# Optimization experiments

Measured on AMD Instinct MI355X. Metric: run time of the kernel, lower is better.

Reference implementation:

```python
import jax, jax.numpy as jnp
import numpy as np

N_NODES = 50000


def setup_inputs() -> dict:
    key = jax.random.key(0)
    k1, k2, k3, k4, k5, k6 = jax.random.split(key, 6)
    N, E, D, F = 50000, 800000, 512, 256
    feature_ori = jax.random.normal(k1, (N, D), dtype=jnp.float32)
    feature_aug = jax.random.normal(k2, (N, D), dtype=jnp.float32)
    edge_row = jax.random.randint(k3, (E,), 0, N, dtype=jnp.int32)
    edge_col = jax.random.randint(k4, (E,), 0, N, dtype=jnp.int32)
    edge_val = jax.random.uniform(k5, (E,), dtype=jnp.float32)
    # kaiming-uniform-ish init for weight, zeros for bias (as in reset_parameters)
    bound = float(np.sqrt(6.0 / D))
    weight = jax.random.uniform(k6, (D, F), dtype=jnp.float32, minval=-bound, maxval=bound)
    bias = jnp.zeros((F,), dtype=jnp.float32)
    return {
        "feature_ori": feature_ori,
        "feature_aug": feature_aug,
        "edge_row": edge_row,
        "edge_col": edge_col,
        "edge_val": edge_val,
        "weight": weight,
        "bias": bias,
    }


def _branch(feat, weight, bias, edge_row, edge_col, edge_val):
    # support = X @ W  -> [N, F]
    support = feat @ weight
    # sparse aggregation: out[i] = sum_{e: row[e]=i} val[e] * support[col[e]]
    msgs = edge_val[:, None] * support[edge_col]          # [E, F]
    out = jax.ops.segment_sum(msgs, edge_row, num_segments=N_NODES)
    return jax.nn.relu(out + bias)


def reference(feature_ori, feature_aug, edge_row, edge_col, edge_val, weight, bias):
    out_ori = _branch(feature_ori, weight, bias, edge_row, edge_col, edge_val)
    out_aug = _branch(feature_aug, weight, bias, edge_row, edge_col, edge_val)
    return (out_ori, out_aug)
```

## Files before the change

### kernel.cpp

```cpp
#include <hip/hip_runtime.h>
#include <hip/hip_bf16.h>

#define NNODES 50000
#define NEDGES 800000
#define DIN    512
#define FOUT   256

typedef __attribute__((ext_vector_type(8))) short short8;
typedef __attribute__((ext_vector_type(4))) float f32x4;
typedef __attribute__((ext_vector_type(4))) unsigned short usv4;

static __device__ __forceinline__ unsigned short f2bf(float f) {
    unsigned int u = __float_as_uint(f);
    u += 0x7FFF + ((u >> 16) & 1);
    return (unsigned short)(u >> 16);
}
static __device__ __forceinline__ float bf2f(unsigned short h) {
    return __uint_as_float(((unsigned int)h) << 16);
}

__global__ void wt_convert(const float* __restrict__ W, unsigned short* __restrict__ Wt) {
    int o = blockIdx.x * 256 + threadIdx.x;
    int n = o >> 9, k = o & 511;
    Wt[o] = f2bf(W[k * FOUT + n]);
}

__global__ void hist_kernel(const int* __restrict__ row, int* __restrict__ cnt) {
    int e = blockIdx.x * 256 + threadIdx.x;
    if (e < NEDGES) atomicAdd(&cnt[row[e]], 1);
}

__global__ void scan_partial(const int* __restrict__ cnt, int* __restrict__ partial) {
    __shared__ int sm[256];
    int i = blockIdx.x * 256 + threadIdx.x;
    int v = (i < NNODES) ? cnt[i] : 0;
    sm[threadIdx.x] = v; __syncthreads();
    for (int s = 128; s > 0; s >>= 1) {
        if (threadIdx.x < s) sm[threadIdx.x] += sm[threadIdx.x + s];
        __syncthreads();
    }
    if (threadIdx.x == 0) partial[blockIdx.x] = sm[0];
}

__global__ void scan_exclusive_small(int* __restrict__ partial, int nb) {
    __shared__ int sm[256];
    int t = threadIdx.x;
    int v = (t < nb) ? partial[t] : 0;
    sm[t] = v; __syncthreads();
    for (int off = 1; off < 256; off <<= 1) {
        int add = (t >= off) ? sm[t - off] : 0;
        __syncthreads();
        sm[t] += add;
        __syncthreads();
    }
    if (t < nb) partial[t] = sm[t] - v;
}

__global__ void scan_write(const int* __restrict__ cnt, const int* __restrict__ partial,
                           int* __restrict__ row_start) {
    __shared__ int sm[256];
    int t = threadIdx.x;
    int i = blockIdx.x * 256 + t;
    int v = (i < NNODES) ? cnt[i] : 0;
    sm[t] = v; __syncthreads();
    for (int off = 1; off < 256; off <<= 1) {
        int add = (t >= off) ? sm[t - off] : 0;
        __syncthreads();
        sm[t] += add;
        __syncthreads();
    }
    if (i < NNODES) row_start[i] = partial[blockIdx.x] + sm[t] - v;
    if (i == 0) row_start[NNODES] = NEDGES;
}

__global__ void scatter_kernel(const int* __restrict__ row, const int* __restrict__ col,
                               const float* __restrict__ val,
                               const int* __restrict__ row_start,
                               int* __restrict__ cursor, unsigned int* __restrict__ cv) {
    int e = blockIdx.x * 256 + threadIdx.x;
    if (e < NEDGES) {
        int r = row[e];
        int pos = atomicAdd(&cursor[r], 1);
        unsigned int vb = f2bf(val[e]);
        cv[row_start[r] + pos] = (vb << 16) | (unsigned int)col[e];
    }
}

__global__ __launch_bounds__(512, 2)
void gemm_kernel(const float* __restrict__ Xo, const float* __restrict__ Xa,
                 const unsigned short* __restrict__ Wt,
                 unsigned short* __restrict__ S) {
    __shared__ __align__(16) unsigned short As[128][40];
    __shared__ __align__(16) unsigned short Bs[256][40];
    const int tid = threadIdx.x;
    const int branch = blockIdx.z;
    const float* __restrict__ X = branch ? Xa : Xo;
    const int boff = branch * 256;
    const int m_base = blockIdx.x * 128;
    const int lane = tid & 63, wave = tid >> 6;
    const int wm = (wave >> 2) * 64, wn = (wave & 3) * 64;
    const int quad = lane >> 4, r16 = lane & 15;

    f32x4 acc[4][4] = {};

    const int colf  = (tid & 7) * 4;
    const int rbase = tid >> 3;
    const int kseg  = (tid & 3) * 8;
    const int nrow  = tid >> 2;

    for (int k0 = 0; k0 < DIN; k0 += 32) {
        #pragma unroll
        for (int i = 0; i < 2; i++) {
            int rr = i * 64 + rbase;
            int gm = m_base + rr;
            float4 v = (gm < NNODES) ? *(const float4*)&X[(long)gm * DIN + k0 + colf]
                                     : make_float4(0.f, 0.f, 0.f, 0.f);
            usv4 h;
            h.x = f2bf(v.x); h.y = f2bf(v.y); h.z = f2bf(v.z); h.w = f2bf(v.w);
            *(usv4*)&As[rr][colf] = h;
        }
        #pragma unroll
        for (int i = 0; i < 2; i++) {
            int nn = i * 128 + nrow;
            *(uint4*)&Bs[nn][kseg] =
                *(const uint4*)&Wt[(long)nn * DIN + k0 + kseg];
        }
        __syncthreads();

        short8 a_frag[4], b_frag[4];
        #pragma unroll
        for (int mi = 0; mi < 4; mi++)
            a_frag[mi] = *(const short8*)&As[wm + mi * 16 + r16][quad * 8];
        #pragma unroll
        for (int ni = 0; ni < 4; ni++)
            b_frag[ni] = *(const short8*)&Bs[wn + ni * 16 + r16][quad * 8];
        #pragma unroll
        for (int mi = 0; mi < 4; mi++)
            #pragma unroll
            for (int ni = 0; ni < 4; ni++)
                acc[mi][ni] = __builtin_amdgcn_mfma_f32_16x16x32_bf16(
                    a_frag[mi], b_frag[ni], acc[mi][ni], 0, 0, 0);
        __syncthreads();
    }

    #pragma unroll
    for (int mi = 0; mi < 4; mi++) {
        #pragma unroll
        for (int rr = 0; rr < 4; rr++) {
            int m = m_base + wm + mi * 16 + quad * 4 + rr;
            if (m < NNODES) {
                #pragma unroll
                for (int ni = 0; ni < 4; ni++) {
                    int n = wn + ni * 16 + r16;
                    S[(long)m * 512 + boff + n] = f2bf(acc[mi][ni][rr]);
                }
            }
        }
    }
}

__global__ __launch_bounds__(256)
void aggregate_kernel(const int* __restrict__ row_start,
                      const unsigned int* __restrict__ cv,
                      const unsigned short* __restrict__ S,
                      const float* __restrict__ bias, float* __restrict__ out) {
    int node = blockIdx.x * 4 + (threadIdx.x >> 6);
    int lane = threadIdx.x & 63;
    if (node >= NNODES) return;
    int s = row_start[node], e = row_start[node + 1];
    float ao0 = 0.f, ao1 = 0.f, ao2 = 0.f, ao3 = 0.f;
    float aa0 = 0.f, aa1 = 0.f, aa2 = 0.f, aa3 = 0.f;
    const int lo = lane * 4;

    int idx = s;
    for (; idx + 4 <= e; idx += 4) {
        unsigned int w0 = cv[idx], w1 = cv[idx + 1], w2 = cv[idx + 2], w3 = cv[idx + 3];
        const unsigned short* p0 = &S[(long)(w0 & 0xFFFFu) * 512 + lo];
        const unsigned short* p1 = &S[(long)(w1 & 0xFFFFu) * 512 + lo];
        const unsigned short* p2 = &S[(long)(w2 & 0xFFFFu) * 512 + lo];
        const unsigned short* p3 = &S[(long)(w3 & 0xFFFFu) * 512 + lo];
        usv4 po0 = *(const usv4*)p0;       usv4 pa0 = *(const usv4*)(p0 + 256);
        usv4 po1 = *(const usv4*)p1;       usv4 pa1 = *(const usv4*)(p1 + 256);
        usv4 po2 = *(const usv4*)p2;       usv4 pa2 = *(const usv4*)(p2 + 256);
        usv4 po3 = *(const usv4*)p3;       usv4 pa3 = *(const usv4*)(p3 + 256);
        float v0 = bf2f((unsigned short)(w0 >> 16));
        float v1 = bf2f((unsigned short)(w1 >> 16));
        float v2 = bf2f((unsigned short)(w2 >> 16));
        float v3 = bf2f((unsigned short)(w3 >> 16));
        ao0 += v0 * bf2f(po0.x); ao1 += v0 * bf2f(po0.y); ao2 += v0 * bf2f(po0.z); ao3 += v0 * bf2f(po0.w);
        aa0 += v0 * bf2f(pa0.x); aa1 += v0 * bf2f(pa0.y); aa2 += v0 * bf2f(pa0.z); aa3 += v0 * bf2f(pa0.w);
        ao0 += v1 * bf2f(po1.x); ao1 += v1 * bf2f(po1.y); ao2 += v1 * bf2f(po1.z); ao3 += v1 * bf2f(po1.w);
        aa0 += v1 * bf2f(pa1.x); aa1 += v1 * bf2f(pa1.y); aa2 += v1 * bf2f(pa1.z); aa3 += v1 * bf2f(pa1.w);
        ao0 += v2 * bf2f(po2.x); ao1 += v2 * bf2f(po2.y); ao2 += v2 * bf2f(po2.z); ao3 += v2 * bf2f(po2.w);
        aa0 += v2 * bf2f(pa2.x); aa1 += v2 * bf2f(pa2.y); aa2 += v2 * bf2f(pa2.z); aa3 += v2 * bf2f(pa2.w);
        ao0 += v3 * bf2f(po3.x); ao1 += v3 * bf2f(po3.y); ao2 += v3 * bf2f(po3.z); ao3 += v3 * bf2f(po3.w);
        aa0 += v3 * bf2f(pa3.x); aa1 += v3 * bf2f(pa3.y); aa2 += v3 * bf2f(pa3.z); aa3 += v3 * bf2f(pa3.w);
    }
    for (; idx < e; idx++) {
        unsigned int w = cv[idx];
        const unsigned short* p = &S[(long)(w & 0xFFFFu) * 512 + lo];
        usv4 po = *(const usv4*)p;
        usv4 pa = *(const usv4*)(p + 256);
        float v = bf2f((unsigned short)(w >> 16));
        ao0 += v * bf2f(po.x); ao1 += v * bf2f(po.y); ao2 += v * bf2f(po.z); ao3 += v * bf2f(po.w);
        aa0 += v * bf2f(pa.x); aa1 += v * bf2f(pa.y); aa2 += v * bf2f(pa.z); aa3 += v * bf2f(pa.w);
    }

    float4 b = *(const float4*)&bias[lo];
    long o = (long)node * FOUT + lo;
    float4 ro, ra;
    ro.x = fmaxf(ao0 + b.x, 0.f); ro.y = fmaxf(ao1 + b.y, 0.f);
    ro.z = fmaxf(ao2 + b.z, 0.f); ro.w = fmaxf(ao3 + b.w, 0.f);
    ra.x = fmaxf(aa0 + b.x, 0.f); ra.y = fmaxf(aa1 + b.y, 0.f);
    ra.z = fmaxf(aa2 + b.z, 0.f); ra.w = fmaxf(aa3 + b.w, 0.f);
    *(float4*)&out[o] = ro;
    *(float4*)&out[(long)NNODES * FOUT + o] = ra;
}

extern "C" void kernel_launch(void* const* d_in, const int* in_sizes, int n_in,
                              void* d_out, int out_size, void* d_ws, size_t ws_size,
                              hipStream_t stream) {
    const float* Xo   = (const float*)d_in[0];
    const float* Xa   = (const float*)d_in[1];
    const int*   erow = (const int*)d_in[2];
    const int*   ecol = (const int*)d_in[3];
    const float* eval_= (const float*)d_in[4];
    const float* W    = (const float*)d_in[5];
    const float* bias = (const float*)d_in[6];
    float* out = (float*)d_out;

    char* ws = (char*)d_ws;
    unsigned short* S         = (unsigned short*)(ws);
    unsigned short* Wt        = (unsigned short*)(ws + 51200000);
    int*            cnt       = (int*)(ws + 51462144);
    int*            row_start = (int*)(ws + 51662144);
    int*            partial   = (int*)(ws + 51862208);
    unsigned int*   cv        = (unsigned int*)(ws + 51863232);

    (void)in_sizes; (void)n_in; (void)out_size; (void)ws_size;

    hipMemsetAsync(cnt, 0, 200000, stream);
    wt_convert<<<512, 256, 0, stream>>>(W, Wt);
    hist_kernel<<<3125, 256, 0, stream>>>(erow, cnt);
    scan_partial<<<196, 256, 0, stream>>>(cnt, partial);
    scan_exclusive_small<<<1, 256, 0, stream>>>(partial, 196);
    scan_write<<<196, 256, 0, stream>>>(cnt, partial, row_start);
    hipMemsetAsync(cnt, 0, 200000, stream);
    scatter_kernel<<<3125, 256, 0, stream>>>(erow, ecol, eval_, row_start, cnt, cv);

    dim3 gg(391, 1, 2);
    gemm_kernel<<<gg, 512, 0, stream>>>(Xo, Xa, Wt, S);

    aggregate_kernel<<<12500, 256, 0, stream>>>(row_start, cv, S, bias, out);
}
```

Measured before the change: 484.2 us.

## Prefetch GEMM tiles in registers, interleave branch layout, and batch aggregate edge loads

```diff
diff --git a/kernel.cpp b/kernel.cpp
--- a/kernel.cpp
+++ b/kernel.cpp
@@ -8,7 +8,6 @@
 
 typedef __attribute__((ext_vector_type(8))) short short8;
 typedef __attribute__((ext_vector_type(4))) float f32x4;
-typedef __attribute__((ext_vector_type(4))) unsigned short usv4;
 
 static __device__ __forceinline__ unsigned short f2bf(float f) {
     unsigned int u = __float_as_uint(f);
@@ -18,16 +17,22 @@
 static __device__ __forceinline__ float bf2f(unsigned short h) {
     return __uint_as_float(((unsigned int)h) << 16);
 }
-
-__global__ void wt_convert(const float* __restrict__ W, unsigned short* __restrict__ Wt) {
-    int o = blockIdx.x * 256 + threadIdx.x;
-    int n = o >> 9, k = o & 511;
-    Wt[o] = f2bf(W[k * FOUT + n]);
-}
-
-__global__ void hist_kernel(const int* __restrict__ row, int* __restrict__ cnt) {
-    int e = blockIdx.x * 256 + threadIdx.x;
-    if (e < NEDGES) atomicAdd(&cnt[row[e]], 1);
+static __device__ __forceinline__ unsigned int pk2bf(float a, float b) {
+    __hip_bfloat162 h = __float22bfloat162_rn(make_float2(a, b));
+    return *(unsigned int*)&h;
+}
+
+__global__ void convert_hist(const float* __restrict__ W, unsigned short* __restrict__ Wt,
+                             const int* __restrict__ row, int* __restrict__ cnt) {
+    int b = blockIdx.x;
+    if (b < 512) {
+        int o = b * 256 + threadIdx.x;
+        int n = o >> 9, k = o & 511;
+        Wt[o] = f2bf(W[k * FOUT + n]);
+    } else {
+        int e = (b - 512) * 256 + threadIdx.x;
+        if (e < NEDGES) atomicAdd(&cnt[row[e]], 1);
+    }
 }
 
 __global__ void scan_partial(const int* __restrict__ cnt, int* __restrict__ partial) {
@@ -56,7 +61,7 @@
     if (t < nb) partial[t] = sm[t] - v;
 }
 
-__global__ void scan_write(const int* __restrict__ cnt, const int* __restrict__ partial,
+__global__ void scan_write(int* __restrict__ cnt, const int* __restrict__ partial,
                            int* __restrict__ row_start) {
     __shared__ int sm[256];
     int t = threadIdx.x;
@@ -69,7 +74,7 @@
         sm[t] += add;
         __syncthreads();
     }
-    if (i < NNODES) row_start[i] = partial[blockIdx.x] + sm[t] - v;
+    if (i < NNODES) { row_start[i] = partial[blockIdx.x] + sm[t] - v; cnt[i] = 0; }
     if (i == 0) row_start[NNODES] = NEDGES;
 }
 
@@ -90,12 +95,11 @@
 void gemm_kernel(const float* __restrict__ Xo, const float* __restrict__ Xa,
                  const unsigned short* __restrict__ Wt,
                  unsigned short* __restrict__ S) {
-    __shared__ __align__(16) unsigned short As[128][40];
-    __shared__ __align__(16) unsigned short Bs[256][40];
+    __shared__ __align__(16) unsigned short As[128][72];
+    __shared__ __align__(16) unsigned short Bs[256][72];
     const int tid = threadIdx.x;
     const int branch = blockIdx.z;
     const float* __restrict__ X = branch ? Xa : Xo;
-    const int boff = branch * 256;
     const int m_base = blockIdx.x * 128;
     const int lane = tid & 63, wave = tid >> 6;
     const int wm = (wave >> 2) * 64, wn = (wave & 3) * 64;
@@ -103,43 +107,72 @@
 
     f32x4 acc[4][4] = {};
 
-    const int colf  = (tid & 7) * 4;
-    const int rbase = tid >> 3;
-    const int kseg  = (tid & 3) * 8;
-    const int nrow  = tid >> 2;
-
-    for (int k0 = 0; k0 < DIN; k0 += 32) {
+    const int scol = (tid & 7) * 8;
+    const int srow = tid >> 3;
+
+    float4 a0[2], a1[2];
+    uint4  breg[4];
+
+    {
         #pragma unroll
         for (int i = 0; i < 2; i++) {
-            int rr = i * 64 + rbase;
-            int gm = m_base + rr;
-            float4 v = (gm < NNODES) ? *(const float4*)&X[(long)gm * DIN + k0 + colf]
-                                     : make_float4(0.f, 0.f, 0.f, 0.f);
-            usv4 h;
-            h.x = f2bf(v.x); h.y = f2bf(v.y); h.z = f2bf(v.z); h.w = f2bf(v.w);
-            *(usv4*)&As[rr][colf] = h;
-        }
+            int gm = m_base + i * 64 + srow;
+            const float* p = &X[(long)gm * DIN + scol];
+            bool ok = gm < NNODES;
+            a0[i] = ok ? *(const float4*)p       : make_float4(0.f,0.f,0.f,0.f);
+            a1[i] = ok ? *(const float4*)(p + 4) : make_float4(0.f,0.f,0.f,0.f);
+        }
+        #pragma unroll
+        for (int i = 0; i < 4; i++)
+            breg[i] = *(const uint4*)&Wt[(long)(i * 64 + srow) * DIN + scol];
+    }
+
+    for (int k0 = 0; k0 < DIN; k0 += 64) {
         #pragma unroll
         for (int i = 0; i < 2; i++) {
-            int nn = i * 128 + nrow;
-            *(uint4*)&Bs[nn][kseg] =
-                *(const uint4*)&Wt[(long)nn * DIN + k0 + kseg];
-        }
-        __syncthreads();
-
-        short8 a_frag[4], b_frag[4];
-        #pragma unroll
-        for (int mi = 0; mi < 4; mi++)
-            a_frag[mi] = *(const short8*)&As[wm + mi * 16 + r16][quad * 8];
-        #pragma unroll
-        for (int ni = 0; ni < 4; ni++)
-            b_frag[ni] = *(const short8*)&Bs[wn + ni * 16 + r16][quad * 8];
-        #pragma unroll
-        for (int mi = 0; mi < 4; mi++)
+            uint4 h;
+            h.x = pk2bf(a0[i].x, a0[i].y);
+            h.y = pk2bf(a0[i].z, a0[i].w);
+            h.z = pk2bf(a1[i].x, a1[i].y);
+            h.w = pk2bf(a1[i].z, a1[i].w);
+            *(uint4*)&As[i * 64 + srow][scol] = h;
+        }
+        #pragma unroll
+        for (int i = 0; i < 4; i++)
+            *(uint4*)&Bs[i * 64 + srow][scol] = breg[i];
+        __syncthreads();
+
+        if (k0 + 64 < DIN) {
+            int k1 = k0 + 64;
+            #pragma unroll
+            for (int i = 0; i < 2; i++) {
+                int gm = m_base + i * 64 + srow;
+                const float* p = &X[(long)gm * DIN + k1 + scol];
+                bool ok = gm < NNODES;
+                a0[i] = ok ? *(const float4*)p       : make_float4(0.f,0.f,0.f,0.f);
+                a1[i] = ok ? *(const float4*)(p + 4) : make_float4(0.f,0.f,0.f,0.f);
+            }
+            #pragma unroll
+            for (int i = 0; i < 4; i++)
+                breg[i] = *(const uint4*)&Wt[(long)(i * 64 + srow) * DIN + k1 + scol];
+        }
+
+        #pragma unroll
+        for (int w = 0; w < 2; w++) {
+            short8 a_frag[4], b_frag[4];
+            #pragma unroll
+            for (int mi = 0; mi < 4; mi++)
+                a_frag[mi] = *(const short8*)&As[wm + mi * 16 + r16][w * 32 + quad * 8];
             #pragma unroll
             for (int ni = 0; ni < 4; ni++)
-                acc[mi][ni] = __builtin_amdgcn_mfma_f32_16x16x32_bf16(
-                    a_frag[mi], b_frag[ni], acc[mi][ni], 0, 0, 0);
+                b_frag[ni] = *(const short8*)&Bs[wn + ni * 16 + r16][w * 32 + quad * 8];
+            #pragma unroll
+            for (int mi = 0; mi < 4; mi++)
+                #pragma unroll
+                for (int ni = 0; ni < 4; ni++)
+                    acc[mi][ni] = __builtin_amdgcn_mfma_f32_16x16x32_bf16(
+                        a_frag[mi], b_frag[ni], acc[mi][ni], 0, 0, 0);
+        }
         __syncthreads();
     }
 
@@ -152,12 +185,19 @@
                 #pragma unroll
                 for (int ni = 0; ni < 4; ni++) {
                     int n = wn + ni * 16 + r16;
-                    S[(long)m * 512 + boff + n] = f2bf(acc[mi][ni][rr]);
+                    int pos = ((n >> 2) * 8) + branch * 4 + (n & 3);
+                    S[(long)m * 512 + pos] = f2bf(acc[mi][ni][rr]);
                 }
             }
         }
     }
 }
+
+#define ACCUM(p, v) { \
+    ao0 += v * __uint_as_float(p.x << 16); ao1 += v * __uint_as_float(p.x & 0xFFFF0000u); \
+    ao2 += v * __uint_as_float(p.y << 16); ao3 += v * __uint_as_float(p.y & 0xFFFF0000u); \
+    aa0 += v * __uint_as_float(p.z << 16); aa1 += v * __uint_as_float(p.z & 0xFFFF0000u); \
+    aa2 += v * __uint_as_float(p.w << 16); aa3 += v * __uint_as_float(p.w & 0xFFFF0000u); }
 
 __global__ __launch_bounds__(256)
 void aggregate_kernel(const int* __restrict__ row_start,
@@ -170,44 +210,37 @@
     int s = row_start[node], e = row_start[node + 1];
     float ao0 = 0.f, ao1 = 0.f, ao2 = 0.f, ao3 = 0.f;
     float aa0 = 0.f, aa1 = 0.f, aa2 = 0.f, aa3 = 0.f;
-    const int lo = lane * 4;
-
-    int idx = s;
-    for (; idx + 4 <= e; idx += 4) {
-        unsigned int w0 = cv[idx], w1 = cv[idx + 1], w2 = cv[idx + 2], w3 = cv[idx + 3];
-        const unsigned short* p0 = &S[(long)(w0 & 0xFFFFu) * 512 + lo];
-        const unsigned short* p1 = &S[(long)(w1 & 0xFFFFu) * 512 + lo];
-        const unsigned short* p2 = &S[(long)(w2 & 0xFFFFu) * 512 + lo];
-        const unsigned short* p3 = &S[(long)(w3 & 0xFFFFu) * 512 + lo];
-        usv4 po0 = *(const usv4*)p0;       usv4 pa0 = *(const usv4*)(p0 + 256);
-        usv4 po1 = *(const usv4*)p1;       usv4 pa1 = *(const usv4*)(p1 + 256);
-        usv4 po2 = *(const usv4*)p2;       usv4 pa2 = *(const usv4*)(p2 + 256);
-        usv4 po3 = *(const usv4*)p3;       usv4 pa3 = *(const usv4*)(p3 + 256);
-        float v0 = bf2f((unsigned short)(w0 >> 16));
-        float v1 = bf2f((unsigned short)(w1 >> 16));
-        float v2 = bf2f((unsigned short)(w2 >> 16));
-        float v3 = bf2f((unsigned short)(w3 >> 16));
-        ao0 += v0 * bf2f(po0.x); ao1 += v0 * bf2f(po0.y); ao2 += v0 * bf2f(po0.z); ao3 += v0 * bf2f(po0.w);
-        aa0 += v0 * bf2f(pa0.x); aa1 += v0 * bf2f(pa0.y); aa2 += v0 * bf2f(pa0.z); aa3 += v0 * bf2f(pa0.w);
-        ao0 += v1 * bf2f(po1.x); ao1 += v1 * bf2f(po1.y); ao2 += v1 * bf2f(po1.z); ao3 += v1 * bf2f(po1.w);
-        aa0 += v1 * bf2f(pa1.x); aa1 += v1 * bf2f(pa1.y); aa2 += v1 * bf2f(pa1.z); aa3 += v1 * bf2f(pa1.w);
-        ao0 += v2 * bf2f(po2.x); ao1 += v2 * bf2f(po2.y); ao2 += v2 * bf2f(po2.z); ao3 += v2 * bf2f(po2.w);
-        aa0 += v2 * bf2f(pa2.x); aa1 += v2 * bf2f(pa2.y); aa2 += v2 * bf2f(pa2.z); aa3 += v2 * bf2f(pa2.w);
-        ao0 += v3 * bf2f(po3.x); ao1 += v3 * bf2f(po3.y); ao2 += v3 * bf2f(po3.z); ao3 += v3 * bf2f(po3.w);
-        aa0 += v3 * bf2f(pa3.x); aa1 += v3 * bf2f(pa3.y); aa2 += v3 * bf2f(pa3.z); aa3 += v3 * bf2f(pa3.w);
-    }
-    for (; idx < e; idx++) {
-        unsigned int w = cv[idx];
-        const unsigned short* p = &S[(long)(w & 0xFFFFu) * 512 + lo];
-        usv4 po = *(const usv4*)p;
-        usv4 pa = *(const usv4*)(p + 256);
-        float v = bf2f((unsigned short)(w >> 16));
-        ao0 += v * bf2f(po.x); ao1 += v * bf2f(po.y); ao2 += v * bf2f(po.z); ao3 += v * bf2f(po.w);
-        aa0 += v * bf2f(pa.x); aa1 += v * bf2f(pa.y); aa2 += v * bf2f(pa.z); aa3 += v * bf2f(pa.w);
-    }
-
-    float4 b = *(const float4*)&bias[lo];
-    long o = (long)node * FOUT + lo;
+    const long rowoff = (long)lane * 8;
+
+    for (int base = s; base < e; base += 64) {
+        int cnt = min(64, e - base);
+        unsigned int cvw = (lane < cnt) ? cv[base + lane] : 0u;
+        int j = 0;
+        for (; j + 4 <= cnt; j += 4) {
+            unsigned int w0 = __shfl(cvw, j);
+            unsigned int w1 = __shfl(cvw, j + 1);
+            unsigned int w2 = __shfl(cvw, j + 2);
+            unsigned int w3 = __shfl(cvw, j + 3);
+            uint4 p0 = *(const uint4*)&S[(long)(w0 & 0xFFFFu) * 512 + rowoff];
+            uint4 p1 = *(const uint4*)&S[(long)(w1 & 0xFFFFu) * 512 + rowoff];
+            uint4 p2 = *(const uint4*)&S[(long)(w2 & 0xFFFFu) * 512 + rowoff];
+            uint4 p3 = *(const uint4*)&S[(long)(w3 & 0xFFFFu) * 512 + rowoff];
+            float v0 = __uint_as_float(w0 & 0xFFFF0000u);
+            float v1 = __uint_as_float(w1 & 0xFFFF0000u);
+            float v2 = __uint_as_float(w2 & 0xFFFF0000u);
+            float v3 = __uint_as_float(w3 & 0xFFFF0000u);
+            ACCUM(p0, v0); ACCUM(p1, v1); ACCUM(p2, v2); ACCUM(p3, v3);
+        }
+        for (; j < cnt; j++) {
+            unsigned int w = __shfl(cvw, j);
+            uint4 p = *(const uint4*)&S[(long)(w & 0xFFFFu) * 512 + rowoff];
+            float v = __uint_as_float(w & 0xFFFF0000u);
+            ACCUM(p, v);
+        }
+    }
+
+    float4 b = *(const float4*)&bias[lane * 4];
+    long o = (long)node * FOUT + lane * 4;
     float4 ro, ra;
     ro.x = fmaxf(ao0 + b.x, 0.f); ro.y = fmaxf(ao1 + b.y, 0.f);
     ro.z = fmaxf(ao2 + b.z, 0.f); ro.w = fmaxf(ao3 + b.w, 0.f);
@@ -240,12 +273,10 @@
     (void)in_sizes; (void)n_in; (void)out_size; (void)ws_size;
 
     hipMemsetAsync(cnt, 0, 200000, stream);
-    wt_convert<<<512, 256, 0, stream>>>(W, Wt);
-    hist_kernel<<<3125, 256, 0, stream>>>(erow, cnt);
+    convert_hist<<<512 + 3125, 256, 0, stream>>>(W, Wt, erow, cnt);
     scan_partial<<<196, 256, 0, stream>>>(cnt, partial);
     scan_exclusive_small<<<1, 256, 0, stream>>>(partial, 196);
     scan_write<<<196, 256, 0, stream>>>(cnt, partial, row_start);
-    hipMemsetAsync(cnt, 0, 200000, stream);
     scatter_kernel<<<3125, 256, 0, stream>>>(erow, ecol, eval_, row_start, cnt, cv);
 
     dim3 gg(391, 1, 2);
```

Result: slower. 536.4 us (+10.8%).
